# Kernel tuning notes

Measured on AMD Instinct MI355X. Metric: run time of the kernel, lower is better.

The kernel has to match this reference:

```python
import jax, jax.numpy as jnp
import numpy as np

B, L = 16, 512          # samples x tokens-per-sample
S = B * L               # total packed tokens
H, HKV, D = 16, 4, 128  # query heads, kv heads, head_dim
G = H // HKV            # GQA group size
HID = 2048
EPS = 1e-6


def rmsnorm(x, w):
    # Qwen2RMSNorm: fp32 variance, scale by weight
    v = jnp.mean(x.astype(jnp.float32) ** 2, axis=-1, keepdims=True)
    return (x.astype(jnp.float32) * jax.lax.rsqrt(v + EPS)).astype(x.dtype) * w


def rotate_half(x):
    x1, x2 = jnp.split(x, 2, axis=-1)
    return jnp.concatenate([-x2, x1], axis=-1)


def setup_inputs() -> dict:
    key = jax.random.key(0)
    ks = jax.random.split(key, 24)
    f = lambda k, shp, s=0.02: (jax.random.normal(k, shp, dtype=jnp.float32) * s)
    inp = {
        'packed_sequence_und': f(ks[0], (S // 2, HID), 1.0),
        'packed_sequence_gen': f(ks[1], (S // 2, HID), 1.0),
        # und tokens on even slots, gen on odd slots -> irregular scatter
        'packed_und_token_indexes': jnp.arange(0, S, 2, dtype=jnp.int32),
        'packed_gen_token_indexes': jnp.arange(1, S, 2, dtype=jnp.int32),
        # und-path projections (q/k/v have bias, o does not)
        'q_w': f(ks[2], (H * D, HID)), 'q_b': f(ks[3], (H * D,)),
        'k_w': f(ks[4], (HKV * D, HID)), 'k_b': f(ks[5], (HKV * D,)),
        'v_w': f(ks[6], (HKV * D, HID)), 'v_b': f(ks[7], (HKV * D,)),
        'o_w': f(ks[8], (HID, H * D)),
        # gen-path (moe_gen) projections
        'q_w_g': f(ks[9], (H * D, HID)), 'q_b_g': f(ks[10], (H * D,)),
        'k_w_g': f(ks[11], (HKV * D, HID)), 'k_b_g': f(ks[12], (HKV * D,)),
        'v_w_g': f(ks[13], (HKV * D, HID)), 'v_b_g': f(ks[14], (HKV * D,)),
        'o_w_g': f(ks[15], (HID, H * D)),
        # qk-norm weights
        'qn_w': jnp.ones((D,), jnp.float32), 'kn_w': jnp.ones((D,), jnp.float32),
        'qn_w_g': jnp.ones((D,), jnp.float32), 'kn_w_g': jnp.ones((D,), jnp.float32),
    }
    # RoPE cos/sin for packed positions (position resets per sample)
    pos = jnp.tile(jnp.arange(L, dtype=jnp.float32), B)            # [S]
    inv_freq = 1.0 / (1e6 ** (jnp.arange(0, D, 2, dtype=jnp.float32) / D))
    freqs = pos[:, None] * inv_freq[None, :]                       # [S, D/2]
    emb = jnp.concatenate([freqs, freqs], axis=-1)                 # [S, D]
    inp['packed_cos'] = jnp.cos(emb)
    inp['packed_sin'] = jnp.sin(emb)
    return inp


def reference(packed_sequence_und, packed_sequence_gen, packed_cos, packed_sin,
              packed_und_token_indexes, packed_gen_token_indexes,
              q_w, q_b, k_w, k_b, v_w, v_b, o_w,
              q_w_g, q_b_g, k_w_g, k_b_g, v_w_g, v_b_g, o_w_g,
              qn_w, kn_w, qn_w_g, kn_w_g):
    ui, gi = packed_und_token_indexes, packed_gen_token_indexes
    # dual-path QKV projection + index scatter into shared packed buffers
    q = jnp.zeros((S, H * D), jnp.float32)
    q = q.at[ui].set(packed_sequence_und @ q_w.T + q_b)
    q = q.at[gi].set(packed_sequence_gen @ q_w_g.T + q_b_g)
    k = jnp.zeros((S, HKV * D), jnp.float32)
    k = k.at[ui].set(packed_sequence_und @ k_w.T + k_b)
    k = k.at[gi].set(packed_sequence_gen @ k_w_g.T + k_b_g)
    v = jnp.zeros((S, HKV * D), jnp.float32)
    v = v.at[ui].set(packed_sequence_und @ v_w.T + v_b)
    v = v.at[gi].set(packed_sequence_gen @ v_w_g.T + v_b_g)

    q = q.reshape(S, H, D)
    k = k.reshape(S, HKV, D)
    v = v.reshape(S, HKV, D)

    # per-stream QK RMSNorm, scattered back
    q = jnp.zeros_like(q).at[ui].set(rmsnorm(q[ui], qn_w)).at[gi].set(rmsnorm(q[gi], qn_w_g))
    k = jnp.zeros_like(k).at[ui].set(rmsnorm(k[ui], kn_w)).at[gi].set(rmsnorm(k[gi], kn_w_g))

    # RoPE (unsqueeze_dim=1)
    cos, sin = packed_cos[:, None, :], packed_sin[:, None, :]
    q = q * cos + rotate_half(q) * sin
    k = k * cos + rotate_half(k) * sin

    # block-diagonal causal attention over packed samples (GQA)
    qb_ = q.reshape(B, L, HKV, G, D)
    kb_ = k.reshape(B, L, HKV, D)
    vb_ = v.reshape(B, L, HKV, D)
    scale = 1.0 / np.sqrt(D)
    scores = jnp.einsum('bqhgd,bkhd->bhgqk', qb_, kb_) * scale   # [B,HKV,G,L,L]
    causal = jnp.tril(jnp.ones((L, L), bool))
    scores = jnp.where(causal, scores, -jnp.inf)
    probs = jax.nn.softmax(scores, axis=-1)
    out = jnp.einsum('bhgqk,bkhd->bqhgd', probs, vb_)            # [B,L,HKV,G,D]
    out = out.reshape(S, H * D)

    out_und = out[ui] @ o_w.T
    out_gen = out[gi] @ o_w_g.T
    return (out_und, out_gen)
```

## Files before the change

kernel.cpp:

```cpp
#include <hip/hip_runtime.h>

typedef __bf16 bf16;
typedef __bf16 bf16x8 __attribute__((ext_vector_type(8)));
typedef float  f32x4  __attribute__((ext_vector_type(4)));

#define HALF   4096
#define S_TOT  8192
#define HID    2048
#define NH     16
#define NKV    4
#define DH     128
#define LSEQ   512

typedef const __attribute__((address_space(1))) void* as1_cvp;
typedef __attribute__((address_space(3))) void* as3_vp;

__device__ __forceinline__ void gl2lds16(const void* g, void* l) {
    __builtin_amdgcn_global_load_lds((as1_cvp)g, (as3_vp)l, 16, 0, 0);
}

__device__ __forceinline__ void hard_barrier() {
    __builtin_amdgcn_sched_barrier(0);
    __builtin_amdgcn_s_barrier();
    __builtin_amdgcn_sched_barrier(0);
}
#define VMCNT(n) asm volatile("s_waitcnt vmcnt(" #n ")" ::: "memory")

struct CvtArgs {
    const float* src[10];
    bf16*        dst[10];
    int          n4[10];
};
__global__ __launch_bounds__(256) void k_convert_multi(CvtArgs a, int total4) {
    int i = blockIdx.x * 256 + threadIdx.x;
    if (i >= total4) return;
    int off = i;
    #pragma unroll
    for (int s = 0; s < 10; ++s) {
        if (off < a.n4[s]) {
            float4 v = ((const float4*)a.src[s])[off];
            union { bf16 b[4]; ushort4 u; } t;
            t.b[0] = (bf16)v.x; t.b[1] = (bf16)v.y; t.b[2] = (bf16)v.z; t.b[3] = (bf16)v.w;
            ((ushort4*)a.dst[s])[off] = t.u;
            return;
        }
        off -= a.n4[s];
    }
}

__global__ void k_invtyp(const int* __restrict__ ui, const int* __restrict__ gi,
                         int* __restrict__ it) {
    int t = blockIdx.x * 256 + threadIdx.x;
    if (t < HALF) { it[ui[t]] = t << 1; it[gi[t]] = (t << 1) | 1; }
}

#define STG2(MB, KC, DST)                                                       \
    gl2lds16((MB) + (KC) + go0, (DST) + wave*1024);                             \
    gl2lds16((MB) + (KC) + go1, (DST) + 8192 + wave*1024);

#define GPHASE(UA, UB, RA, RB, DO_B, NOFF, NMH, MH, STG, TAIL)                  \
  {                                                                             \
    _Pragma("unroll")                                                           \
    for (int im = 0; im < 4; ++im)                                              \
        RA[im] = *(const bf16x8*)(sAb + (NOFF) + (NMH)*4096 + im*1024 + abase); \
    if (DO_B) {                                                                 \
        _Pragma("unroll")                                                       \
        for (int jn = 0; jn < 4; ++jn)                                          \
            RB[jn] = *(const bf16x8*)(sBb + (NOFF) + jn*1024 + bbase);          \
    }                                                                           \
    STG;                                                                        \
    __builtin_amdgcn_s_setprio(1);                                              \
    _Pragma("unroll")                                                           \
    for (int im = 0; im < 4; ++im)                                              \
      _Pragma("unroll")                                                         \
      for (int jn = 0; jn < 4; ++jn)                                            \
        acc[(MH)*4+im][jn] = __builtin_amdgcn_mfma_f32_16x16x32_bf16(           \
            UA[im], UB[jn], acc[(MH)*4+im][jn], 0, 0, 0);                       \
    __builtin_amdgcn_s_setprio(0);                                              \
    TAIL;                                                                       \
    hard_barrier();                                                             \
  }

__device__ __forceinline__ void gemm256_core(
    const bf16* __restrict__ A, const bf16* __restrict__ B,
    int m0, int n0, int tid, char* sAb, char* sBb, f32x4 (&acc)[8][4])
{
    const int lane = tid & 63;
    const int lm = lane & 15, kq = lane >> 4;
    const int wave = tid >> 6;
    const int wm = wave >> 2, wn = wave & 3;

    const int swz16 = (kq ^ ((lm >> 1) & 3)) * 16;
    const int abase = wm*8192 + lm*64 + swz16;
    const int bbase = wn*4096 + lm*64 + swz16;

    int go0, go1;
    {
        const int s0 = tid,        r0 = s0 >> 2, c0 = (s0 & 3) ^ ((r0 >> 1) & 3);
        const int s1 = 512 + tid,  r1 = s1 >> 2, c1 = (s1 & 3) ^ ((r1 >> 1) & 3);
        go0 = r0*HID + c0*8;
        go1 = r1*HID + c1*8;
    }
    const bf16* Ab = A + (size_t)m0*HID;
    const bf16* Bb = B + (size_t)n0*HID;

    bf16x8 afA[4], afB[4], bfA[4], bfB[4];

    STG2(Ab, 0,  sAb + 0);      STG2(Ab, 32, sAb + 16384);
    STG2(Bb, 0,  sBb + 0);      STG2(Bb, 32, sBb + 16384);
    STG2(Ab, 64, sAb + 32768);  STG2(Bb, 64, sBb + 32768);
    VMCNT(4);
    hard_barrier();
    #pragma unroll
    for (int im = 0; im < 4; ++im) afA[im] = *(const bf16x8*)(sAb + im*1024 + abase);
    #pragma unroll
    for (int jn = 0; jn < 4; ++jn) bfA[jn] = *(const bf16x8*)(sBb + jn*1024 + bbase);

    #pragma unroll 1
    for (int i = 0; i < 15; ++i) {
        const int kc = 128*i;
        GPHASE(afA,bfA, afB,bfA, 0, 0,     1, 0, STG2(Ab, kc+96,  sAb+49152), VMCNT(6));
        GPHASE(afB,bfA, afA,bfB, 1, 16384, 0, 1, STG2(Bb, kc+96,  sBb+49152), (void)0);
        GPHASE(afA,bfB, afB,bfA, 0, 16384, 1, 0, STG2(Ab, kc+128, sAb+0),     VMCNT(6));
        GPHASE(afB,bfB, afA,bfA, 1, 32768, 0, 1, STG2(Bb, kc+128, sBb+0),     (void)0);
        GPHASE(afA,bfA, afB,bfA, 0, 32768, 1, 0, STG2(Ab, kc+160, sAb+16384), VMCNT(6));
        GPHASE(afB,bfA, afA,bfB, 1, 49152, 0, 1, STG2(Bb, kc+160, sBb+16384), (void)0);
        GPHASE(afA,bfB, afB,bfA, 0, 49152, 1, 0, STG2(Ab, kc+192, sAb+32768), VMCNT(6));
        GPHASE(afB,bfB, afA,bfA, 1, 0,     0, 1, STG2(Bb, kc+192, sBb+32768), (void)0);
    }
    {
        GPHASE(afA,bfA, afB,bfA, 0, 0,     1, 0, STG2(Ab, 2016, sAb+49152), VMCNT(6));
        GPHASE(afB,bfA, afA,bfB, 1, 16384, 0, 1, STG2(Bb, 2016, sBb+49152), (void)0);
        GPHASE(afA,bfB, afB,bfA, 0, 16384, 1, 0, (void)0,                   VMCNT(4));
        GPHASE(afB,bfB, afA,bfA, 1, 32768, 0, 1, (void)0,                   (void)0);
        GPHASE(afA,bfA, afB,bfA, 0, 32768, 1, 0, (void)0,                   VMCNT(0));
        GPHASE(afB,bfA, afA,bfB, 1, 49152, 0, 1, (void)0,                   (void)0);
        GPHASE(afA,bfB, afB,bfA, 0, 49152, 1, 0, (void)0,                   (void)0);
        GPHASE(afB,bfB, afA,bfA, 1, 0,     0, 1, (void)0,                   (void)0);
    }
}

__global__ __launch_bounds__(512, 2) void k_gemm_qkv(
    const bf16* __restrict__ Xu, const bf16* __restrict__ Xg,
    const bf16* __restrict__ Wu, const bf16* __restrict__ Wg,
    const float* __restrict__ qbu, const float* __restrict__ kbu, const float* __restrict__ vbu,
    const float* __restrict__ qbg, const float* __restrict__ kbg, const float* __restrict__ vbg,
    const int* __restrict__ ui, const int* __restrict__ gi,
    bf16* __restrict__ qo, bf16* __restrict__ ko, bf16* __restrict__ vo)
{
    __shared__ __align__(16) bf16 sA[2][2][256*32];
    __shared__ __align__(16) bf16 sB[2][2][256*32];

    const int gen = blockIdx.z;
    const bf16* X = gen ? Xg : Xu;
    const bf16* W = gen ? Wg : Wu;
    const float* qb = gen ? qbg : qbu;
    const float* kb = gen ? kbg : kbu;
    const float* vb = gen ? vbg : vbu;
    const int* idx = gen ? gi : ui;

    const int tid = threadIdx.x;
    const int wave = tid >> 6, lane = tid & 63;
    const int lm = lane & 15, kq = lane >> 4;
    const int wm = wave >> 2, wn = wave & 3;
    const int m0 = blockIdx.y * 256, n0 = blockIdx.x * 256;

    f32x4 acc[8][4] = {};
    gemm256_core(X, W, m0, n0, tid, (char*)&sA[0][0][0], (char*)&sB[0][0][0], acc);

    #pragma unroll
    for (int im = 0; im < 8; ++im) {
        int srow[4];
        #pragma unroll
        for (int r = 0; r < 4; ++r) srow[r] = idx[m0 + wm*128 + im*16 + kq*4 + r];
        #pragma unroll
        for (int jn = 0; jn < 4; ++jn) {
            const int o = n0 + wn*64 + jn*16 + lm;
            bf16* dst; float bias; int off0, ld;
            if (o < 2048)      { dst = qo; ld = 2048; off0 = o;        bias = qb[o]; }
            else if (o < 2560) { dst = ko; ld = 512;  off0 = o - 2048; bias = kb[o-2048]; }
            else               { dst = vo; ld = 512;  off0 = o - 2560; bias = vb[o-2560]; }
            #pragma unroll
            for (int r = 0; r < 4; ++r)
                dst[(size_t)srow[r]*ld + off0] = (bf16)(acc[im][jn][r] + bias);
        }
    }
}

__global__ __launch_bounds__(256) void k_norm_rope(
    bf16* __restrict__ qbuf, bf16* __restrict__ kbuf,
    const float* __restrict__ cosb, const float* __restrict__ sinb,
    const int* __restrict__ invtyp,
    const float* __restrict__ qnu, const float* __restrict__ qng,
    const float* __restrict__ knu, const float* __restrict__ kng)
{
    const int row = blockIdx.x * 4 + (threadIdx.x >> 6);
    const int lane = threadIdx.x & 63;
    const int s = row / (NH + NKV), hh = row % (NH + NKV);
    const int isg = invtyp[s] & 1;
    bf16* ptr; const float* w; float qs;
    if (hh < NH) { ptr = qbuf + (size_t)s*HID + hh*DH;           w = isg ? qng : qnu;
                   qs = 0.08838834764831845f * 1.4426950408889634f; }
    else         { ptr = kbuf + (size_t)s*(NKV*DH) + (hh-NH)*DH; w = isg ? kng : knu;
                   qs = 1.0f; }

    const unsigned u = *(const unsigned*)((const unsigned short*)ptr + 2*lane);
    const float f0 = __uint_as_float(u << 16);
    const float f1 = __uint_as_float(u & 0xffff0000u);
    float ss = f0*f0 + f1*f1;
    #pragma unroll
    for (int m = 32; m; m >>= 1) ss += __shfl_xor(ss, m, 64);
    const float r = rsqrtf(ss * (1.0f/128.0f) + 1e-6f);
    const float2 wv = *(const float2*)(w + 2*lane);
    const float xn0 = f0 * r * wv.x;
    const float xn1 = f1 * r * wv.y;
    const float po0 = __shfl_xor(xn0, 32, 64);
    const float po1 = __shfl_xor(xn1, 32, 64);
    const float2 c2 = *(const float2*)(cosb + (size_t)s*DH + 2*lane);
    const float2 s2 = *(const float2*)(sinb + (size_t)s*DH + 2*lane);
    const float sg = (lane < 32) ? -1.0f : 1.0f;
    const float o0 = (xn0 * c2.x + sg * po0 * s2.x) * qs;
    const float o1 = (xn1 * c2.y + sg * po1 * s2.y) * qs;
    union { unsigned short us[2]; unsigned u; } t;
    bf16 b0 = (bf16)o0, b1 = (bf16)o1;
    t.us[0] = *(unsigned short*)&b0; t.us[1] = *(unsigned short*)&b1;
    *(unsigned*)((unsigned short*)ptr + 2*lane) = t.u;
}

__global__ __launch_bounds__(256) void k_vtrans(const bf16* __restrict__ v, bf16* __restrict__ vt)
{
    __shared__ __align__(16) bf16 sT[64 * 132];
    const int kvh = blockIdx.y;
    const int s0 = blockIdx.x * 64;
    const int b = s0 >> 9;
    const int pos0 = s0 & 511;
    const int tid = threadIdx.x;

    #pragma unroll
    for (int i = 0; i < 4; ++i) {
        const int c = i*256 + tid;
        const int rowi = c >> 4, col8 = c & 15;
        const uint4 d = *(const uint4*)(v + (size_t)(s0 + rowi)*(NKV*DH) + kvh*DH + col8*8);
        uint2* lp = (uint2*)&sT[rowi*132 + col8*8];
        lp[0] = make_uint2(d.x, d.y);
        lp[1] = make_uint2(d.z, d.w);
    }
    __syncthreads();
    const int dd = tid >> 1, half = tid & 1;
    __align__(16) bf16 tmp[32];
    #pragma unroll
    for (int p = 0; p < 32; ++p) tmp[p] = sT[(half*32 + p)*132 + dd];
    bf16* dst = vt + ((size_t)(b*NKV + kvh)*DH + dd)*LSEQ + pos0 + half*32;
    #pragma unroll
    for (int q = 0; q < 8; ++q) ((ushort4*)dst)[q] = ((ushort4*)tmp)[q];
}

__global__ __launch_bounds__(256) void k_attn(
    const bf16* __restrict__ qbuf, const bf16* __restrict__ kbuf,
    const bf16* __restrict__ vt, const int* __restrict__ invtyp,
    bf16* __restrict__ aop_u, bf16* __restrict__ aop_g)
{
    __shared__ __align__(16) bf16 sK[2][64*128];
    __shared__ __align__(16) bf16 sV[2][128*64];
    __shared__ __align__(16) bf16 sP[4][16*72];

    const int qt = 7 - blockIdx.x;
    const int h = blockIdx.y, b = blockIdx.z;
    const int kvh = h >> 2;
    const int tid = threadIdx.x, wave = tid >> 6, lane = tid & 63;
    const int lm = lane & 15, kq = lane >> 4;
    const int q0 = qt * 64;

    bf16x8 qfrag[4];
    {
        const bf16* qp = qbuf + ((size_t)(b*LSEQ + q0 + wave*16 + lm))*HID + h*DH;
        #pragma unroll
        for (int ks = 0; ks < 4; ++ks)
            qfrag[ks] = *(const bf16x8*)(qp + ks*32 + kq*8);
    }

    const bf16* kbase = kbuf + ((size_t)(b*LSEQ))*(NKV*DH) + kvh*DH;
    const bf16* vbase = vt + ((size_t)(b*NKV + kvh)*DH)*LSEQ;

    f32x4 accO[8] = {};
    float lpart[4] = {0.f, 0.f, 0.f, 0.f};
    bf16* const sPw = &sP[wave][0];

    {
        const bf16* kp = kbase;
        const bf16* vp = vbase;
        #pragma unroll
        for (int i = 0; i < 4; ++i) {
            const int g = i*4 + wave;
            const int ch = g*64 + lane;
            { const int row = ch >> 4, cp = ch & 15;
              const int c = (cp & 8) | ((cp ^ row) & 7);
              gl2lds16(kp + (size_t)row*(NKV*DH) + c*8, (char*)&sK[0][0] + (size_t)g*1024); }
            { const int d = ch >> 3, cp = ch & 7;
              const int c = (cp ^ d) & 7;
              gl2lds16(vp + (size_t)d*LSEQ + c*8, (char*)&sV[0][0] + (size_t)g*1024); }
        }
    }

    for (int kt = 0; kt <= qt; ++kt) {
        const int cur = kt & 1;
        __syncthreads();

        if (kt < qt) {
            const bf16* kp = kbase + (size_t)((kt+1)*64)*(NKV*DH);
            const bf16* vp = vbase + (kt+1)*64;
            const int nxt = cur ^ 1;
            #pragma unroll
            for (int i = 0; i < 4; ++i) {
                const int g = i*4 + wave;
                const int ch = g*64 + lane;
                { const int row = ch >> 4, cp = ch & 15;
                  const int c = (cp & 8) | ((cp ^ row) & 7);
                  gl2lds16(kp + (size_t)row*(NKV*DH) + c*8, (char*)&sK[nxt][0] + (size_t)g*1024); }
                { const int d = ch >> 3, cp = ch & 7;
                  const int c = (cp ^ d) & 7;
                  gl2lds16(vp + (size_t)d*LSEQ + c*8, (char*)&sV[nxt][0] + (size_t)g*1024); }
            }
        }

        f32x4 s4[4] = {};
        #pragma unroll
        for (int ks = 0; ks < 4; ++ks) {
            const int cq = ks*4 + kq;
            const int cs = (cq & 8) | ((cq ^ lm) & 7);
            #pragma unroll
            for (int nt = 0; nt < 4; ++nt) {
                bf16x8 bk = *(const bf16x8*)&sK[cur][(nt*16 + lm)*128 + cs*8];
                s4[nt] = __builtin_amdgcn_mfma_f32_16x16x32_bf16(qfrag[ks], bk, s4[nt], 0, 0, 0);
            }
        }

        const bool diag = (kt == qt);
        #pragma unroll
        for (int r = 0; r < 4; ++r) {
            const int rloc = wave*16 + kq*4 + r;
            float v0 = s4[0][r], v1 = s4[1][r], v2 = s4[2][r], v3 = s4[3][r];
            if (diag) {
                if (lm      > rloc) v0 = -1e30f;
                if (lm + 16 > rloc) v1 = -1e30f;
                if (lm + 32 > rloc) v2 = -1e30f;
                if (lm + 48 > rloc) v3 = -1e30f;
            }
            const float p0 = exp2f(v0);
            const float p1 = exp2f(v1);
            const float p2 = exp2f(v2);
            const float p3 = exp2f(v3);
            lpart[r] += (p0 + p1) + (p2 + p3);
            const int prow = (kq*4 + r) * 72;
            sPw[prow + lm]      = (bf16)p0;
            sPw[prow + 16 + lm] = (bf16)p1;
            sPw[prow + 32 + lm] = (bf16)p2;
            sPw[prow + 48 + lm] = (bf16)p3;
        }

        #pragma unroll
        for (int pc = 0; pc < 2; ++pc) {
            bf16x8 ap = *(const bf16x8*)&sPw[lm*72 + pc*32 + kq*8];
            #pragma unroll
            for (int dt = 0; dt < 8; ++dt) {
                const int cv = (pc*4 + kq);
                const int cs = (cv ^ lm) & 7;
                bf16x8 bv = *(const bf16x8*)&sV[cur][(dt*16 + lm)*64 + cs*8];
                accO[dt] = __builtin_amdgcn_mfma_f32_16x16x32_bf16(ap, bv, accO[dt], 0, 0, 0);
            }
        }
    }

    #pragma unroll
    for (int r = 0; r < 4; ++r) {
        float l = lpart[r];
        l += __shfl_xor(l, 1, 64);
        l += __shfl_xor(l, 2, 64);
        l += __shfl_xor(l, 4, 64);
        l += __shfl_xor(l, 8, 64);
        const int srow = b*LSEQ + q0 + wave*16 + kq*4 + r;
        const int code = invtyp[srow];
        bf16* dst = (code & 1) ? aop_g : aop_u;
        const size_t off = (size_t)(code >> 1)*HID + h*DH;
        const float inv_l = 1.0f / l;
        #pragma unroll
        for (int dt = 0; dt < 8; ++dt)
            dst[off + dt*16 + lm] = (bf16)(accO[dt][r] * inv_l);
    }
}

__global__ __launch_bounds__(512, 2) void k_gemm_out(
    const bf16* __restrict__ Au, const bf16* __restrict__ Ag,
    const bf16* __restrict__ Wu, const bf16* __restrict__ Wg,
    float* __restrict__ out)
{
    __shared__ __align__(16) bf16 sA[2][2][256*32];
    __shared__ __align__(16) bf16 sB[2][2][256*32];

    const int gen = blockIdx.z;
    const bf16* A = gen ? Ag : Au;
    const bf16* W = gen ? Wg : Wu;
    float* O = out + (size_t)gen * HALF * HID;

    const int tid = threadIdx.x;
    const int wave = tid >> 6, lane = tid & 63;
    const int lm = lane & 15, kq = lane >> 4;
    const int wm = wave >> 2, wn = wave & 3;
    const int m0 = blockIdx.y * 256, n0 = blockIdx.x * 256;

    f32x4 acc[8][4] = {};
    gemm256_core(A, W, m0, n0, tid, (char*)&sA[0][0][0], (char*)&sB[0][0][0], acc);

    #pragma unroll
    for (int im = 0; im < 8; ++im)
        #pragma unroll
        for (int jn = 0; jn < 4; ++jn)
            #pragma unroll
            for (int r = 0; r < 4; ++r)
                O[(size_t)(m0 + wm*128 + im*16 + kq*4 + r)*HID + (n0 + wn*64 + jn*16 + lm)]
                    = acc[im][jn][r];
}

extern "C" void kernel_launch(void* const* d_in, const int* in_sizes, int n_in,
                              void* d_out, int out_size, void* d_ws, size_t ws_size,
                              hipStream_t stream)
{
    (void)in_sizes; (void)n_in; (void)out_size; (void)ws_size;
    const float* x_u  = (const float*)d_in[0];
    const float* x_g  = (const float*)d_in[1];
    const int*   ui   = (const int*)d_in[2];
    const int*   gi   = (const int*)d_in[3];
    const float* q_w  = (const float*)d_in[4];
    const float* q_b  = (const float*)d_in[5];
    const float* k_w  = (const float*)d_in[6];
    const float* k_b  = (const float*)d_in[7];
    const float* v_w  = (const float*)d_in[8];
    const float* v_b  = (const float*)d_in[9];
    const float* o_w  = (const float*)d_in[10];
    const float* q_wg = (const float*)d_in[11];
    const float* q_bg = (const float*)d_in[12];
    const float* k_wg = (const float*)d_in[13];
    const float* k_bg = (const float*)d_in[14];
    const float* v_wg = (const float*)d_in[15];
    const float* v_bg = (const float*)d_in[16];
    const float* o_wg = (const float*)d_in[17];
    const float* qn_u = (const float*)d_in[18];
    const float* kn_u = (const float*)d_in[19];
    const float* qn_g = (const float*)d_in[20];
    const float* kn_g = (const float*)d_in[21];
    const float* cosb = (const float*)d_in[22];
    const float* sinb = (const float*)d_in[23];

    char* w = (char*)d_ws;
    auto alloc = [&](size_t bytes) { char* p = w; w += (bytes + 255) & ~(size_t)255; return p; };
    bf16* xb_u   = (bf16*)alloc((size_t)HALF*HID*2);
    bf16* xb_g   = (bf16*)alloc((size_t)HALF*HID*2);
    bf16* wqkv_u = (bf16*)alloc((size_t)3072*HID*2);
    bf16* wqkv_g = (bf16*)alloc((size_t)3072*HID*2);
    bf16* wo_u   = (bf16*)alloc((size_t)HID*HID*2);
    bf16* wo_g   = (bf16*)alloc((size_t)HID*HID*2);
    bf16* qbuf   = (bf16*)alloc((size_t)S_TOT*HID*2);
    bf16* kbuf   = (bf16*)alloc((size_t)S_TOT*NKV*DH*2);
    bf16* vbuf   = (bf16*)alloc((size_t)S_TOT*NKV*DH*2);
    bf16* vtb    = (bf16*)alloc((size_t)S_TOT*NKV*DH*2);
    int*  invtyp = (int*)alloc((size_t)S_TOT*4);
    bf16* aop_u = xb_u;
    bf16* aop_g = xb_g;

    CvtArgs ca;
    int total4 = 0, si = 0;
    auto seg = [&](const float* s, bf16* d, size_t n) {
        ca.src[si] = s; ca.dst[si] = d; ca.n4[si] = (int)(n / 4);
        total4 += (int)(n / 4); ++si;
    };
    seg(x_u,  xb_u,                (size_t)HALF*HID);
    seg(x_g,  xb_g,                (size_t)HALF*HID);
    seg(q_w,  wqkv_u,              (size_t)2048*HID);
    seg(k_w,  wqkv_u + 2048*HID,   (size_t)512*HID);
    seg(v_w,  wqkv_u + 2560*HID,   (size_t)512*HID);
    seg(q_wg, wqkv_g,              (size_t)2048*HID);
    seg(k_wg, wqkv_g + 2048*HID,   (size_t)512*HID);
    seg(v_wg, wqkv_g + 2560*HID,   (size_t)512*HID);
    seg(o_w,  wo_u,                (size_t)HID*HID);
    seg(o_wg, wo_g,                (size_t)HID*HID);
    k_convert_multi<<<(total4 + 255)/256, 256, 0, stream>>>(ca, total4);

    k_invtyp<<<16, 256, 0, stream>>>(ui, gi, invtyp);

    k_gemm_qkv<<<dim3(12, 16, 2), 512, 0, stream>>>(
        xb_u, xb_g, wqkv_u, wqkv_g,
        q_b, k_b, v_b, q_bg, k_bg, v_bg,
        ui, gi, qbuf, kbuf, vbuf);

    k_norm_rope<<<(S_TOT*(NH+NKV))/4, 256, 0, stream>>>(
        qbuf, kbuf, cosb, sinb, invtyp, qn_u, qn_g, kn_u, kn_g);

    k_vtrans<<<dim3(S_TOT/64, NKV), 256, 0, stream>>>(vbuf, vtb);

    k_attn<<<dim3(LSEQ/64, NH, 16), 256, 0, stream>>>(
        qbuf, kbuf, vtb, invtyp, aop_u, aop_g);

    k_gemm_out<<<dim3(8, 16, 2), 512, 0, stream>>>(
        aop_u, aop_g, wo_u, wo_g, (float*)d_out);
}
```

Baseline: 540.9 us.

## Rework GEMM LDS pipeline to single-register phases and XCD-aware block remap

```diff
diff --git a/kernel.cpp b/kernel.cpp
--- a/kernel.cpp
+++ b/kernel.cpp
@@ -19,11 +19,6 @@
     __builtin_amdgcn_global_load_lds((as1_cvp)g, (as3_vp)l, 16, 0, 0);
 }
 
-__device__ __forceinline__ void hard_barrier() {
-    __builtin_amdgcn_sched_barrier(0);
-    __builtin_amdgcn_s_barrier();
-    __builtin_amdgcn_sched_barrier(0);
-}
 #define VMCNT(n) asm volatile("s_waitcnt vmcnt(" #n ")" ::: "memory")
 
 struct CvtArgs {
@@ -54,31 +49,37 @@
     if (t < HALF) { it[ui[t]] = t << 1; it[gi[t]] = (t << 1) | 1; }
 }
 
+#define C0 0
+#define C1 16384
+#define C2 32768
+#define C3 49152
+
 #define STG2(MB, KC, DST)                                                       \
     gl2lds16((MB) + (KC) + go0, (DST) + wave*1024);                             \
     gl2lds16((MB) + (KC) + go1, (DST) + 8192 + wave*1024);
 
-#define GPHASE(UA, UB, RA, RB, DO_B, NOFF, NMH, MH, STG, TAIL)                  \
+#define PH(RD, MH, DOB, STG, TAIL)                                              \
   {                                                                             \
     _Pragma("unroll")                                                           \
     for (int im = 0; im < 4; ++im)                                              \
-        RA[im] = *(const bf16x8*)(sAb + (NOFF) + (NMH)*4096 + im*1024 + abase); \
-    if (DO_B) {                                                                 \
+        a_[im] = *(const bf16x8*)(sAb + (RD) + (MH)*4096 + im*1024 + abase);    \
+    if (DOB) {                                                                  \
         _Pragma("unroll")                                                       \
         for (int jn = 0; jn < 4; ++jn)                                          \
-            RB[jn] = *(const bf16x8*)(sBb + (NOFF) + jn*1024 + bbase);          \
+            b_[jn] = *(const bf16x8*)(sBb + (RD) + jn*1024 + bbase);            \
     }                                                                           \
     STG;                                                                        \
+    __builtin_amdgcn_s_barrier();                                               \
     __builtin_amdgcn_s_setprio(1);                                              \
     _Pragma("unroll")                                                           \
     for (int im = 0; im < 4; ++im)                                              \
       _Pragma("unroll")                                                         \
       for (int jn = 0; jn < 4; ++jn)                                            \
         acc[(MH)*4+im][jn] = __builtin_amdgcn_mfma_f32_16x16x32_bf16(           \
-            UA[im], UB[jn], acc[(MH)*4+im][jn], 0, 0, 0);                       \
+            a_[im], b_[jn], acc[(MH)*4+im][jn], 0, 0, 0);                       \
     __builtin_amdgcn_s_setprio(0);                                              \
     TAIL;                                                                       \
-    hard_barrier();                                                             \
+    __builtin_amdgcn_s_barrier();                                               \
   }
 
 __device__ __forceinline__ void gemm256_core(
@@ -104,39 +105,35 @@
     const bf16* Ab = A + (size_t)m0*HID;
     const bf16* Bb = B + (size_t)n0*HID;
 
-    bf16x8 afA[4], afB[4], bfA[4], bfB[4];
-
-    STG2(Ab, 0,  sAb + 0);      STG2(Ab, 32, sAb + 16384);
-    STG2(Bb, 0,  sBb + 0);      STG2(Bb, 32, sBb + 16384);
-    STG2(Ab, 64, sAb + 32768);  STG2(Bb, 64, sBb + 32768);
+    bf16x8 a_[4], b_[4];
+
+    STG2(Ab, 0,  sAb + C0);  STG2(Ab, 32, sAb + C1);
+    STG2(Bb, 0,  sBb + C0);  STG2(Bb, 32, sBb + C1);
+    STG2(Ab, 64, sAb + C2);  STG2(Bb, 64, sBb + C2);
     VMCNT(4);
-    hard_barrier();
-    #pragma unroll
-    for (int im = 0; im < 4; ++im) afA[im] = *(const bf16x8*)(sAb + im*1024 + abase);
-    #pragma unroll
-    for (int jn = 0; jn < 4; ++jn) bfA[jn] = *(const bf16x8*)(sBb + jn*1024 + bbase);
+    __builtin_amdgcn_s_barrier();
 
     #pragma unroll 1
     for (int i = 0; i < 15; ++i) {
         const int kc = 128*i;
-        GPHASE(afA,bfA, afB,bfA, 0, 0,     1, 0, STG2(Ab, kc+96,  sAb+49152), VMCNT(6));
-        GPHASE(afB,bfA, afA,bfB, 1, 16384, 0, 1, STG2(Bb, kc+96,  sBb+49152), (void)0);
-        GPHASE(afA,bfB, afB,bfA, 0, 16384, 1, 0, STG2(Ab, kc+128, sAb+0),     VMCNT(6));
-        GPHASE(afB,bfB, afA,bfA, 1, 32768, 0, 1, STG2(Bb, kc+128, sBb+0),     (void)0);
-        GPHASE(afA,bfA, afB,bfA, 0, 32768, 1, 0, STG2(Ab, kc+160, sAb+16384), VMCNT(6));
-        GPHASE(afB,bfA, afA,bfB, 1, 49152, 0, 1, STG2(Bb, kc+160, sBb+16384), (void)0);
-        GPHASE(afA,bfB, afB,bfA, 0, 49152, 1, 0, STG2(Ab, kc+192, sAb+32768), VMCNT(6));
-        GPHASE(afB,bfB, afA,bfA, 1, 0,     0, 1, STG2(Bb, kc+192, sBb+32768), (void)0);
+        PH(C0, 0, 1, STG2(Ab, kc+96,  sAb+C3), (void)0);
+        PH(C0, 1, 0, STG2(Bb, kc+96,  sBb+C3), (void)0);
+        PH(C1, 0, 1, STG2(Ab, kc+128, sAb+C0), (void)0);
+        PH(C1, 1, 0, STG2(Bb, kc+128, sBb+C0), VMCNT(4));
+        PH(C2, 0, 1, STG2(Ab, kc+160, sAb+C1), (void)0);
+        PH(C2, 1, 0, STG2(Bb, kc+160, sBb+C1), (void)0);
+        PH(C3, 0, 1, STG2(Ab, kc+192, sAb+C2), (void)0);
+        PH(C3, 1, 0, STG2(Bb, kc+192, sBb+C2), VMCNT(4));
     }
     {
-        GPHASE(afA,bfA, afB,bfA, 0, 0,     1, 0, STG2(Ab, 2016, sAb+49152), VMCNT(6));
-        GPHASE(afB,bfA, afA,bfB, 1, 16384, 0, 1, STG2(Bb, 2016, sBb+49152), (void)0);
-        GPHASE(afA,bfB, afB,bfA, 0, 16384, 1, 0, (void)0,                   VMCNT(4));
-        GPHASE(afB,bfB, afA,bfA, 1, 32768, 0, 1, (void)0,                   (void)0);
-        GPHASE(afA,bfA, afB,bfA, 0, 32768, 1, 0, (void)0,                   VMCNT(0));
-        GPHASE(afB,bfA, afA,bfB, 1, 49152, 0, 1, (void)0,                   (void)0);
-        GPHASE(afA,bfB, afB,bfA, 0, 49152, 1, 0, (void)0,                   (void)0);
-        GPHASE(afB,bfB, afA,bfA, 1, 0,     0, 1, (void)0,                   (void)0);
+        PH(C0, 0, 1, STG2(Ab, 2016, sAb+C3), (void)0);
+        PH(C0, 1, 0, STG2(Bb, 2016, sBb+C3), (void)0);
+        PH(C1, 0, 1, (void)0, (void)0);
+        PH(C1, 1, 0, (void)0, VMCNT(0));
+        PH(C2, 0, 1, (void)0, (void)0);
+        PH(C2, 1, 0, (void)0, (void)0);
+        PH(C3, 0, 1, (void)0, (void)0);
+        PH(C3, 1, 0, (void)0, (void)0);
     }
 }
 
@@ -148,31 +145,37 @@
     const int* __restrict__ ui, const int* __restrict__ gi,
     bf16* __restrict__ qo, bf16* __restrict__ ko, bf16* __restrict__ vo)
 {
-    __shared__ __align__(16) bf16 sA[2][2][256*32];
-    __shared__ __align__(16) bf16 sB[2][2][256*32];
-
-    const int gen = blockIdx.z;
+    __shared__ __align__(16) bf16 sA[4][256*32];
+    __shared__ __align__(16) bf16 sB[4][256*32];
+
+    const int lin = blockIdx.x;
+    const int idx = (lin & 7) * 48 + (lin >> 3);
+    const int gen = idx / 192;
+    const int rem = idx - gen * 192;
+    const int my  = rem / 12;
+    const int nx_ = rem - my * 12;
+    const int m0 = my * 256, n0 = nx_ * 256;
+
     const bf16* X = gen ? Xg : Xu;
     const bf16* W = gen ? Wg : Wu;
     const float* qb = gen ? qbg : qbu;
     const float* kb = gen ? kbg : kbu;
     const float* vb = gen ? vbg : vbu;
-    const int* idx = gen ? gi : ui;
+    const int* idxmap = gen ? gi : ui;
 
     const int tid = threadIdx.x;
     const int wave = tid >> 6, lane = tid & 63;
     const int lm = lane & 15, kq = lane >> 4;
     const int wm = wave >> 2, wn = wave & 3;
-    const int m0 = blockIdx.y * 256, n0 = blockIdx.x * 256;
 
     f32x4 acc[8][4] = {};
-    gemm256_core(X, W, m0, n0, tid, (char*)&sA[0][0][0], (char*)&sB[0][0][0], acc);
+    gemm256_core(X, W, m0, n0, tid, (char*)&sA[0][0], (char*)&sB[0][0], acc);
 
     #pragma unroll
     for (int im = 0; im < 8; ++im) {
         int srow[4];
         #pragma unroll
-        for (int r = 0; r < 4; ++r) srow[r] = idx[m0 + wm*128 + im*16 + kq*4 + r];
+        for (int r = 0; r < 4; ++r) srow[r] = idxmap[m0 + wm*128 + im*16 + kq*4 + r];
         #pragma unroll
         for (int jn = 0; jn < 4; ++jn) {
             const int o = n0 + wn*64 + jn*16 + lm;
@@ -394,10 +397,17 @@
     const bf16* __restrict__ Wu, const bf16* __restrict__ Wg,
     float* __restrict__ out)
 {
-    __shared__ __align__(16) bf16 sA[2][2][256*32];
-    __shared__ __align__(16) bf16 sB[2][2][256*32];
-
-    const int gen = blockIdx.z;
+    __shared__ __align__(16) bf16 sA[4][256*32];
+    __shared__ __align__(16) bf16 sB[4][256*32];
+
+    const int lin = blockIdx.x;
+    const int idx = (lin & 7) * 32 + (lin >> 3);
+    const int gen = idx / 128;
+    const int rem = idx - gen * 128;
+    const int my  = rem >> 3;
+    const int nx_ = rem & 7;
+    const int m0 = my * 256, n0 = nx_ * 256;
+
     const bf16* A = gen ? Ag : Au;
     const bf16* W = gen ? Wg : Wu;
     float* O = out + (size_t)gen * HALF * HID;
@@ -406,10 +416,9 @@
     const int wave = tid >> 6, lane = tid & 63;
     const int lm = lane & 15, kq = lane >> 4;
     const int wm = wave >> 2, wn = wave & 3;
-    const int m0 = blockIdx.y * 256, n0 = blockIdx.x * 256;
 
     f32x4 acc[8][4] = {};
-    gemm256_core(A, W, m0, n0, tid, (char*)&sA[0][0][0], (char*)&sB[0][0][0], acc);
+    gemm256_core(A, W, m0, n0, tid, (char*)&sA[0][0], (char*)&sB[0][0], acc);
 
     #pragma unroll
     for (int im = 0; im < 8; ++im)
@@ -487,7 +496,7 @@
 
     k_invtyp<<<16, 256, 0, stream>>>(ui, gi, invtyp);
 
-    k_gemm_qkv<<<dim3(12, 16, 2), 512, 0, stream>>>(
+    k_gemm_qkv<<<dim3(384), 512, 0, stream>>>(
         xb_u, xb_g, wqkv_u, wqkv_g,
         q_b, k_b, v_b, q_bg, k_bg, v_bg,
         ui, gi, qbuf, kbuf, vbuf);
@@ -500,6 +509,6 @@
     k_attn<<<dim3(LSEQ/64, NH, 16), 256, 0, stream>>>(
         qbuf, kbuf, vtb, invtyp, aop_u, aop_g);
 
-    k_gemm_out<<<dim3(8, 16, 2), 512, 0, stream>>>(
+    k_gemm_out<<<dim3(256), 512, 0, stream>>>(
         aop_u, aop_g, wo_u, wo_g, (float*)d_out);
 }
```

Result: faster. 525.9 us (-2.8%).
